# Optimization experiments

Hardware: AMD Instinct MI355X
Metric: run time of the kernel (lower is better)

## Reference

```python
import jax, jax.numpy as jnp
import numpy as np

N_NODES = 500_000
MEM_DIM = 256
MSG_DIM = 256
N_UPD = 100_000


def setup_inputs() -> dict:
    key = jax.random.key(0)
    ks = jax.random.split(key, 10)
    s = 1.0 / np.sqrt(MEM_DIM)
    return {
        "unique_node_ids": jnp.arange(N_UPD, dtype=jnp.int64)
        if jax.config.jax_enable_x64 else jnp.arange(N_UPD, dtype=jnp.int32),
        "unique_messages": jax.random.normal(ks[0], (N_UPD, MSG_DIM), jnp.float32),
        "timestamps": jax.random.uniform(ks[1], (N_UPD,), jnp.float32),
        "net_transaction_amounts": jax.random.normal(ks[2], (N_UPD,), jnp.float32),
        "memory": jax.random.normal(ks[3], (N_NODES, MEM_DIM), jnp.float32),
        "last_update": jnp.zeros((N_NODES,), jnp.float32),
        "W_cat": jax.random.normal(ks[4], (MEM_DIM, MSG_DIM + 1), jnp.float32) * s,
        "b_cat": jnp.zeros((MEM_DIM,), jnp.float32),
        "W_ih": jax.random.normal(ks[5], (3 * MEM_DIM, MEM_DIM), jnp.float32) * s,
        "W_hh": jax.random.normal(ks[6], (3 * MEM_DIM, MEM_DIM), jnp.float32) * s,
        "b_ih": jnp.zeros((3 * MEM_DIM,), jnp.float32),
        "b_hh": jnp.zeros((3 * MEM_DIM,), jnp.float32),
    }


def _gru_cell(x, h, W_ih, W_hh, b_ih, b_hh):
    # torch.nn.GRUCell math
    gi = x @ W_ih.T + b_ih      # [N, 3*D]
    gh = h @ W_hh.T + b_hh      # [N, 3*D]
    i_r, i_z, i_n = jnp.split(gi, 3, axis=1)
    h_r, h_z, h_n = jnp.split(gh, 3, axis=1)
    r = jax.nn.sigmoid(i_r + h_r)
    z = jax.nn.sigmoid(i_z + h_z)
    n = jnp.tanh(i_n + r * h_n)
    return (1.0 - z) * n + z * h


def reference(unique_node_ids, unique_messages, timestamps, net_transaction_amounts,
              memory, last_update, W_cat, b_cat, W_ih, W_hh, b_ih, b_hh):
    # concat message with scalar amount, small linear projection
    cat = jnp.concatenate([unique_messages, net_transaction_amounts[:, None]], axis=1)
    final_inputs = cat @ W_cat.T + b_cat                # [N_upd, MEM_DIM]
    h = memory[unique_node_ids]                         # gather by id
    new_h = _gru_cell(final_inputs, h, W_ih, W_hh, b_ih, b_hh)
    updated_memory = memory.at[unique_node_ids].set(new_h)        # scatter back
    updated_last_update = last_update.at[unique_node_ids].set(timestamps)
    return updated_memory, updated_last_update
```

## Files before the change

kernel.cpp:

```cpp
#include <hip/hip_runtime.h>
#include <hip/hip_bf16.h>

typedef __attribute__((ext_vector_type(8))) short s16x8;
typedef __attribute__((ext_vector_type(4))) float f32x4;

__device__ __forceinline__ unsigned short f2bf(float x) {
    unsigned int u = __float_as_uint(x);
    u += 0x7fffu + ((u >> 16) & 1u);
    return (unsigned short)(u >> 16);
}
__device__ __forceinline__ float bf2f(unsigned short h) {
    return __uint_as_float((unsigned int)h << 16);
}
__device__ __forceinline__ void gload_lds16(const void* g, void* l) {
    __builtin_amdgcn_global_load_lds(
        (const __attribute__((address_space(1))) void*)g,
        (__attribute__((address_space(3))) void*)(unsigned int)(size_t)l,
        16, 0, 0);
}

__global__ void prep_w_kernel(const float* __restrict__ W_cat,
                              const float* __restrict__ b_cat,
                              const float* __restrict__ W_ih,
                              const float* __restrict__ W_hh,
                              const float* __restrict__ b_ih,
                              unsigned short* __restrict__ wm,
                              unsigned short* __restrict__ whh,
                              float* __restrict__ wamt,
                              float* __restrict__ bcomb) {
    int idx = blockIdx.x * blockDim.x + threadIdx.x;
    const int NW = 768 * 256;
    if (idx < NW) {
        int g = idx >> 8, c = idx & 255;
        float s = 0.f;
        #pragma unroll 4
        for (int k = 0; k < 256; ++k) s += W_ih[g * 256 + k] * W_cat[k * 257 + c];
        wm[idx] = f2bf(s);
    } else if (idx < 2 * NW) {
        int t = idx - NW;
        whh[t] = f2bf(W_hh[t]);
    } else if (idx < 2 * NW + 768) {
        int g = idx - 2 * NW;
        float sa = 0.f, sb = 0.f;
        for (int k = 0; k < 256; ++k) {
            float w = W_ih[g * 256 + k];
            sa += w * W_cat[k * 257 + 256];
            sb += w * b_cat[k];
        }
        wamt[g] = sa;
        bcomb[g] = sb + b_ih[g];
    }
}

__global__ void prep_msgs_kernel(const float* __restrict__ msgs,
                                 unsigned short* __restrict__ mbf,
                                 const float* __restrict__ lu,
                                 float* __restrict__ out_lu,
                                 long mchunks, long luchunks) {
    long stride = (long)gridDim.x * blockDim.x;
    long total = mchunks + luchunks;
    for (long i = blockIdx.x * (long)blockDim.x + threadIdx.x; i < total; i += stride) {
        if (i < mchunks) {
            const float4* s = (const float4*)(msgs + i * 8);
            float4 a = s[0], b = s[1];
            s16x8 v = { (short)f2bf(a.x), (short)f2bf(a.y), (short)f2bf(a.z), (short)f2bf(a.w),
                        (short)f2bf(b.x), (short)f2bf(b.y), (short)f2bf(b.z), (short)f2bf(b.w) };
            *(s16x8*)(mbf + i * 8) = v;
        } else {
            long j = i - mchunks;
            ((float4*)out_lu)[j] = ((const float4*)lu)[j];
        }
    }
}

__global__ void build_inv_kernel(const int* __restrict__ ids, int* __restrict__ inv, int M) {
    int i = blockIdx.x * blockDim.x + threadIdx.x;
    if (i < M) inv[ids[i]] = i + 1;
}

template<bool HBF>
__global__ void copy_gather_kernel(const float* __restrict__ memory,
                                   const int* __restrict__ inv,
                                   float* __restrict__ out_mem,
                                   unsigned short* __restrict__ hbf,
                                   int N) {
    int wave = (blockIdx.x * blockDim.x + threadIdx.x) >> 6;
    int lane = threadIdx.x & 63;
    int nw = (gridDim.x * blockDim.x) >> 6;
    for (int row = wave; row < N; row += nw) {
        int iv = inv[row];
        if (iv == 0) {
            float4 v = ((const float4*)(memory + (size_t)row * 256))[lane];
            ((float4*)(out_mem + (size_t)row * 256))[lane] = v;
        } else if (HBF) {
            float4 v = ((const float4*)(memory + (size_t)row * 256))[lane];
            ushort4 o = { f2bf(v.x), f2bf(v.y), f2bf(v.z), f2bf(v.w) };
            *(ushort4*)(hbf + (size_t)(iv - 1) * 256 + lane * 4) = o;
        }
    }
}

__device__ __forceinline__ void stage_dma_a(const unsigned short* __restrict__ base,
                                            int m0, int M, int k0, char* ldsbuf, int tid) {
    #pragma unroll
    for (int it = 0; it < 2; ++it) {
        int q = tid + it * 512;
        int row = q >> 3;
        int part = (q & 7) ^ (row & 7);
        int grow = m0 + row; if (grow >= M) grow = M - 1;
        gload_lds16((const char*)base + (size_t)grow * 512 + k0 * 2 + part * 16,
                    ldsbuf + (tid & ~63) * 16 + it * 8192);
    }
}
__device__ __forceinline__ void stage_dma_w(const unsigned short* __restrict__ wm,
                                            const unsigned short* __restrict__ whh,
                                            int nc, int k0, char* swbuf, int tid) {
    #pragma unroll
    for (int it = 0; it < 6; ++it) {
        int q = tid + it * 512;
        int r = q >> 3;
        int part = (q & 7) ^ (r & 7);
        int pn = r >> 6, rr = r & 63;
        const unsigned short* src = (pn < 3)
            ? wm  + ((size_t)(pn * 256 + nc * 64 + rr)) * 256
            : whh + ((size_t)((pn - 3) * 256 + nc * 64 + rr)) * 256;
        gload_lds16((const char*)src + k0 * 2 + part * 16,
                    swbuf + (tid & ~63) * 16 + it * 8192);
    }
}
__device__ __forceinline__ void stage_reg_h(const int* __restrict__ ids,
                                            const float* __restrict__ memory,
                                            int m0, int M, int k0, char* shbuf, int tid) {
    #pragma unroll
    for (int it = 0; it < 2; ++it) {
        int q = tid + it * 512;
        int row = q >> 3, part = q & 7;
        int grow = m0 + row; if (grow >= M) grow = M - 1;
        int gid = ids[grow];
        const float4* src = (const float4*)(memory + (size_t)gid * 256 + k0 + part * 8);
        float4 a = src[0], b = src[1];
        s16x8 v = { (short)f2bf(a.x), (short)f2bf(a.y), (short)f2bf(a.z), (short)f2bf(a.w),
                    (short)f2bf(b.x), (short)f2bf(b.y), (short)f2bf(b.z), (short)f2bf(b.w) };
        *(s16x8*)(shbuf + row * 128 + ((part ^ (row & 7)) * 16)) = v;
    }
}

template<bool HBF>
__global__ __launch_bounds__(512, 2)
void gru_kernel(const int* __restrict__ ids,
                const unsigned short* __restrict__ mbf,
                const unsigned short* __restrict__ hbf,
                const float* __restrict__ memory,
                const unsigned short* __restrict__ wm,
                const unsigned short* __restrict__ whh,
                const float* __restrict__ wamt,
                const float* __restrict__ bcomb,
                const float* __restrict__ b_hh,
                const float* __restrict__ amt,
                const float* __restrict__ ts,
                float* __restrict__ out_mem,
                float* __restrict__ out_lu,
                int M, int mtiles) {
    extern __shared__ char lds[];

    int g = blockIdx.x;
    int xcd = g & 7, s = g >> 3;
    int nc = s & 3;
    int mtile = (s >> 2) * 8 + xcd;
    if (mtile >= mtiles) return;
    int m0 = mtile * 128;

    int tid = threadIdx.x;
    int lane = tid & 63;
    int w = tid >> 6;
    int wr = w >> 2, wc = w & 3;

    stage_dma_a(mbf, m0, M, 0, lds, tid);
    if (HBF) stage_dma_a(hbf, m0, M, 0, lds + 32768, tid);
    else     stage_reg_h(ids, memory, m0, M, 0, lds + 32768, tid);
    stage_dma_w(wm, whh, nc, 0, lds + 65536, tid);
    __syncthreads();

    f32x4 acc[6][4];
    #pragma unroll
    for (int pn = 0; pn < 6; ++pn)
        #pragma unroll
        for (int mf = 0; mf < 4; ++mf) acc[pn][mf] = (f32x4){0.f, 0.f, 0.f, 0.f};

    #pragma unroll
    for (int ks = 0; ks < 4; ++ks) {
        char* sm = lds + ((ks & 1) << 14);
        char* sh = lds + 32768 + ((ks & 1) << 14);
        char* sw = lds + 65536 + (ks & 1) * 49152;
        if (ks < 3) {
            int k0 = (ks + 1) * 64;
            char* smn = lds + (((ks + 1) & 1) << 14);
            char* shn = lds + 32768 + (((ks + 1) & 1) << 14);
            char* swn = lds + 65536 + ((ks + 1) & 1) * 49152;
            stage_dma_a(mbf, m0, M, k0, smn, tid);
            if (HBF) stage_dma_a(hbf, m0, M, k0, shn, tid);
            else     stage_reg_h(ids, memory, m0, M, k0, shn, tid);
            stage_dma_w(wm, whh, nc, k0, swn, tid);
        }
        #pragma unroll
        for (int c = 0; c < 2; ++c) {
            int p = c * 4 + (lane >> 4);
            s16x8 ax[4], ah[4], bw[6];
            #pragma unroll
            for (int mf = 0; mf < 4; ++mf) {
                int row = wr * 64 + mf * 16 + (lane & 15);
                int off = row * 128 + ((p ^ (row & 7)) * 16);
                ax[mf] = *(const s16x8*)(sm + off);
                ah[mf] = *(const s16x8*)(sh + off);
            }
            #pragma unroll
            for (int pn = 0; pn < 6; ++pn) {
                int r = pn * 64 + wc * 16 + (lane & 15);
                bw[pn] = *(const s16x8*)(sw + r * 128 + ((p ^ (r & 7)) * 16));
            }
            #pragma unroll
            for (int pn = 0; pn < 6; ++pn)
                #pragma unroll
                for (int mf = 0; mf < 4; ++mf)
                    acc[pn][mf] = __builtin_amdgcn_mfma_f32_16x16x32_bf16(
                        (pn < 3) ? ax[mf] : ah[mf], bw[pn], acc[pn][mf], 0, 0, 0);
        }
        __syncthreads();
    }

    int colL = wc * 16 + (lane & 15);
    int col = nc * 64 + colL;
    float bi0 = bcomb[col], bi1 = bcomb[256 + col], bi2 = bcomb[512 + col];
    float bh0 = b_hh[col],  bh1 = b_hh[256 + col],  bh2 = b_hh[512 + col];
    float wa0 = wamt[col],  wa1 = wamt[256 + col],  wa2 = wamt[512 + col];
    bool lu_thread = (nc == 0) && (colL == 0);
    #pragma unroll
    for (int mf = 0; mf < 4; ++mf) {
        int rb = wr * 64 + mf * 16 + (lane >> 4) * 4;
        #pragma unroll
        for (int r = 0; r < 4; ++r) {
            int grow = m0 + rb + r; if (grow >= M) grow = M - 1;
            int gid = ids[grow];
            float amtv = amt[grow];
            float hv = HBF ? bf2f(hbf[(size_t)grow * 256 + col])
                           : memory[(size_t)gid * 256 + col];
            float ir = acc[0][mf][r] + bi0 + amtv * wa0;
            float iz = acc[1][mf][r] + bi1 + amtv * wa1;
            float in_ = acc[2][mf][r] + bi2 + amtv * wa2;
            float hr = acc[3][mf][r] + bh0;
            float hz = acc[4][mf][r] + bh1;
            float hn = acc[5][mf][r] + bh2;
            float rg = 1.f / (1.f + __expf(-(ir + hr)));
            float zg = 1.f / (1.f + __expf(-(iz + hz)));
            float ng = tanhf(in_ + rg * hn);
            out_mem[(size_t)gid * 256 + col] = (1.f - zg) * ng + zg * hv;
            if (lu_thread) out_lu[gid] = ts[grow];
        }
    }
}

extern "C" void kernel_launch(void* const* d_in, const int* in_sizes, int n_in,
                              void* d_out, int out_size, void* d_ws, size_t ws_size,
                              hipStream_t stream) {
    const int*   ids   = (const int*)  d_in[0];
    const float* msgs  = (const float*)d_in[1];
    const float* ts    = (const float*)d_in[2];
    const float* amt   = (const float*)d_in[3];
    const float* mem   = (const float*)d_in[4];
    const float* lu    = (const float*)d_in[5];
    const float* W_cat = (const float*)d_in[6];
    const float* b_cat = (const float*)d_in[7];
    const float* W_ih  = (const float*)d_in[8];
    const float* W_hh  = (const float*)d_in[9];
    const float* b_ih  = (const float*)d_in[10];
    const float* b_hh  = (const float*)d_in[11];

    int M = in_sizes[0];
    int N = in_sizes[5];

    float* out_mem = (float*)d_out;
    float* out_lu  = out_mem + (size_t)N * 256;

    char* ws = (char*)d_ws;
    unsigned short* wm    = (unsigned short*)ws;
    unsigned short* whh   = wm + 768 * 256;
    float*          wamt  = (float*)(whh + 768 * 256);
    float*          bcomb = wamt + 768;
    int*            inv   = (int*)(bcomb + 768);
    size_t off_mbf = (((char*)(inv + N) - ws) + 15) & ~(size_t)15;
    unsigned short* mbf   = (unsigned short*)(ws + off_mbf);
    unsigned short* hbf   = (unsigned short*)(ws + off_mbf + (size_t)M * 512);
    size_t need_hbf = off_mbf + 2 * (size_t)M * 512;
    bool use_hbf = ws_size >= need_hbf;

    prep_w_kernel<<<(2 * 768 * 256 + 768 + 255) / 256, 256, 0, stream>>>(
        W_cat, b_cat, W_ih, W_hh, b_ih, wm, whh, wamt, bcomb);

    long mchunks = (long)M * 32;
    long luchunks = N / 4;
    prep_msgs_kernel<<<2048, 256, 0, stream>>>(msgs, mbf, lu, out_lu, mchunks, luchunks);

    (void)hipMemsetAsync(inv, 0, (size_t)N * 4, stream);
    build_inv_kernel<<<(M + 255) / 256, 256, 0, stream>>>(ids, inv, M);

    int mtiles = (M + 127) / 128;
    int mt8 = ((mtiles + 7) / 8) * 8;

    if (use_hbf) {
        copy_gather_kernel<true><<<2048, 256, 0, stream>>>(mem, inv, out_mem, hbf, N);
        (void)hipFuncSetAttribute((const void*)gru_kernel<true>,
                                  hipFuncAttributeMaxDynamicSharedMemorySize, 163840);
        gru_kernel<true><<<mt8 * 4, 512, 163840, stream>>>(
            ids, mbf, hbf, mem, wm, whh, wamt, bcomb, b_hh, amt, ts,
            out_mem, out_lu, M, mtiles);
    } else {
        copy_gather_kernel<false><<<2048, 256, 0, stream>>>(mem, inv, out_mem, hbf, N);
        (void)hipFuncSetAttribute((const void*)gru_kernel<false>,
                                  hipFuncAttributeMaxDynamicSharedMemorySize, 163840);
        gru_kernel<false><<<mt8 * 4, 512, 163840, stream>>>(
            ids, mbf, hbf, mem, wm, whh, wamt, bcomb, b_hh, amt, ts,
            out_mem, out_lu, M, mtiles);
    }
}
```

Measured before the change: 454.8 us.

## Fuse bf16 conversion into GRU kernel loads and drop bf16 staging buffers

Removes the separate message and hidden-state bf16 pre-conversion passes (prep_msgs and the hbf write in copy_gather). The GRU kernel now loads fp32 messages and gathered memory rows directly into registers, converts them, and writes them to single-buffered LDS between two barriers, while weights keep the DMA double buffer. The copy of untouched rows and the last_update write move to a copy kernel that runs after the GRU kernel, with 4-way unrolled row loads. A cheaper exp-based tanh replaces tanhf. This cuts a full extra round trip through HBM for the staged bf16 arrays, at the cost of an extra barrier per k-step and less load/compute overlap for the activation tiles.

```diff
diff --git a/kernel.cpp b/kernel.cpp
--- a/kernel.cpp
+++ b/kernel.cpp
@@ -9,14 +9,19 @@
     u += 0x7fffu + ((u >> 16) & 1u);
     return (unsigned short)(u >> 16);
 }
-__device__ __forceinline__ float bf2f(unsigned short h) {
-    return __uint_as_float((unsigned int)h << 16);
+__device__ __forceinline__ s16x8 pack8(float4 a, float4 b) {
+    return (s16x8){ (short)f2bf(a.x), (short)f2bf(a.y), (short)f2bf(a.z), (short)f2bf(a.w),
+                    (short)f2bf(b.x), (short)f2bf(b.y), (short)f2bf(b.z), (short)f2bf(b.w) };
 }
 __device__ __forceinline__ void gload_lds16(const void* g, void* l) {
     __builtin_amdgcn_global_load_lds(
         (const __attribute__((address_space(1))) void*)g,
         (__attribute__((address_space(3))) void*)(unsigned int)(size_t)l,
         16, 0, 0);
+}
+__device__ __forceinline__ float sigf(float x) { return 1.f / (1.f + __expf(-x)); }
+__device__ __forceinline__ float tanhfast(float x) {
+    return 1.f - 2.f / (__expf(2.f * x) + 1.f);
 }
 
 __global__ void prep_w_kernel(const float* __restrict__ W_cat,
@@ -52,69 +57,14 @@
     }
 }
 
-__global__ void prep_msgs_kernel(const float* __restrict__ msgs,
-                                 unsigned short* __restrict__ mbf,
-                                 const float* __restrict__ lu,
-                                 float* __restrict__ out_lu,
-                                 long mchunks, long luchunks) {
-    long stride = (long)gridDim.x * blockDim.x;
-    long total = mchunks + luchunks;
-    for (long i = blockIdx.x * (long)blockDim.x + threadIdx.x; i < total; i += stride) {
-        if (i < mchunks) {
-            const float4* s = (const float4*)(msgs + i * 8);
-            float4 a = s[0], b = s[1];
-            s16x8 v = { (short)f2bf(a.x), (short)f2bf(a.y), (short)f2bf(a.z), (short)f2bf(a.w),
-                        (short)f2bf(b.x), (short)f2bf(b.y), (short)f2bf(b.z), (short)f2bf(b.w) };
-            *(s16x8*)(mbf + i * 8) = v;
-        } else {
-            long j = i - mchunks;
-            ((float4*)out_lu)[j] = ((const float4*)lu)[j];
-        }
-    }
-}
-
 __global__ void build_inv_kernel(const int* __restrict__ ids, int* __restrict__ inv, int M) {
     int i = blockIdx.x * blockDim.x + threadIdx.x;
     if (i < M) inv[ids[i]] = i + 1;
 }
 
-template<bool HBF>
-__global__ void copy_gather_kernel(const float* __restrict__ memory,
-                                   const int* __restrict__ inv,
-                                   float* __restrict__ out_mem,
-                                   unsigned short* __restrict__ hbf,
-                                   int N) {
-    int wave = (blockIdx.x * blockDim.x + threadIdx.x) >> 6;
-    int lane = threadIdx.x & 63;
-    int nw = (gridDim.x * blockDim.x) >> 6;
-    for (int row = wave; row < N; row += nw) {
-        int iv = inv[row];
-        if (iv == 0) {
-            float4 v = ((const float4*)(memory + (size_t)row * 256))[lane];
-            ((float4*)(out_mem + (size_t)row * 256))[lane] = v;
-        } else if (HBF) {
-            float4 v = ((const float4*)(memory + (size_t)row * 256))[lane];
-            ushort4 o = { f2bf(v.x), f2bf(v.y), f2bf(v.z), f2bf(v.w) };
-            *(ushort4*)(hbf + (size_t)(iv - 1) * 256 + lane * 4) = o;
-        }
-    }
-}
-
-__device__ __forceinline__ void stage_dma_a(const unsigned short* __restrict__ base,
-                                            int m0, int M, int k0, char* ldsbuf, int tid) {
-    #pragma unroll
-    for (int it = 0; it < 2; ++it) {
-        int q = tid + it * 512;
-        int row = q >> 3;
-        int part = (q & 7) ^ (row & 7);
-        int grow = m0 + row; if (grow >= M) grow = M - 1;
-        gload_lds16((const char*)base + (size_t)grow * 512 + k0 * 2 + part * 16,
-                    ldsbuf + (tid & ~63) * 16 + it * 8192);
-    }
-}
-__device__ __forceinline__ void stage_dma_w(const unsigned short* __restrict__ wm,
-                                            const unsigned short* __restrict__ whh,
-                                            int nc, int k0, char* swbuf, int tid) {
+__device__ __forceinline__ void dma_w(const unsigned short* __restrict__ wm,
+                                      const unsigned short* __restrict__ whh,
+                                      int nc, int k0, char* swbuf, int tid) {
     #pragma unroll
     for (int it = 0; it < 6; ++it) {
         int q = tid + it * 512;
@@ -128,28 +78,10 @@
                     swbuf + (tid & ~63) * 16 + it * 8192);
     }
 }
-__device__ __forceinline__ void stage_reg_h(const int* __restrict__ ids,
-                                            const float* __restrict__ memory,
-                                            int m0, int M, int k0, char* shbuf, int tid) {
-    #pragma unroll
-    for (int it = 0; it < 2; ++it) {
-        int q = tid + it * 512;
-        int row = q >> 3, part = q & 7;
-        int grow = m0 + row; if (grow >= M) grow = M - 1;
-        int gid = ids[grow];
-        const float4* src = (const float4*)(memory + (size_t)gid * 256 + k0 + part * 8);
-        float4 a = src[0], b = src[1];
-        s16x8 v = { (short)f2bf(a.x), (short)f2bf(a.y), (short)f2bf(a.z), (short)f2bf(a.w),
-                    (short)f2bf(b.x), (short)f2bf(b.y), (short)f2bf(b.z), (short)f2bf(b.w) };
-        *(s16x8*)(shbuf + row * 128 + ((part ^ (row & 7)) * 16)) = v;
-    }
-}
-
-template<bool HBF>
+
 __global__ __launch_bounds__(512, 2)
 void gru_kernel(const int* __restrict__ ids,
-                const unsigned short* __restrict__ mbf,
-                const unsigned short* __restrict__ hbf,
+                const float* __restrict__ msgs,
                 const float* __restrict__ memory,
                 const unsigned short* __restrict__ wm,
                 const unsigned short* __restrict__ whh,
@@ -157,11 +89,13 @@
                 const float* __restrict__ bcomb,
                 const float* __restrict__ b_hh,
                 const float* __restrict__ amt,
-                const float* __restrict__ ts,
                 float* __restrict__ out_mem,
-                float* __restrict__ out_lu,
                 int M, int mtiles) {
     extern __shared__ char lds[];
+    char* sm  = lds;
+    char* sh  = lds + 16384;
+    char* sw0 = lds + 32768;
+    char* sw1 = lds + 81920;
 
     int g = blockIdx.x;
     int xcd = g & 7, s = g >> 3;
@@ -175,10 +109,29 @@
     int w = tid >> 6;
     int wr = w >> 2, wc = w & 3;
 
-    stage_dma_a(mbf, m0, M, 0, lds, tid);
-    if (HBF) stage_dma_a(hbf, m0, M, 0, lds + 32768, tid);
-    else     stage_reg_h(ids, memory, m0, M, 0, lds + 32768, tid);
-    stage_dma_w(wm, whh, nc, 0, lds + 65536, tid);
+    int row0 = tid >> 3, row1 = (tid + 512) >> 3;
+    int part = tid & 7;
+    int gr0 = m0 + row0; if (gr0 >= M) gr0 = M - 1;
+    int gr1 = m0 + row1; if (gr1 >= M) gr1 = M - 1;
+    const float* mp0 = msgs + (size_t)gr0 * 256 + part * 8;
+    const float* mp1 = msgs + (size_t)gr1 * 256 + part * 8;
+    const float* hp0 = memory + (size_t)ids[gr0] * 256 + part * 8;
+    const float* hp1 = memory + (size_t)ids[gr1] * 256 + part * 8;
+    int ld0 = row0 * 128 + ((part ^ (row0 & 7)) * 16);
+    int ld1 = row1 * 128 + ((part ^ (row1 & 7)) * 16);
+
+    float4 ma0, mb0, ma1, mb1, ha0, hb0, ha1, hb1;
+    {
+        ma0 = *(const float4*)(mp0);     mb0 = *(const float4*)(mp0 + 4);
+        ma1 = *(const float4*)(mp1);     mb1 = *(const float4*)(mp1 + 4);
+        ha0 = *(const float4*)(hp0);     hb0 = *(const float4*)(hp0 + 4);
+        ha1 = *(const float4*)(hp1);     hb1 = *(const float4*)(hp1 + 4);
+        dma_w(wm, whh, nc, 0, sw0, tid);
+        *(s16x8*)(sm + ld0) = pack8(ma0, mb0);
+        *(s16x8*)(sm + ld1) = pack8(ma1, mb1);
+        *(s16x8*)(sh + ld0) = pack8(ha0, hb0);
+        *(s16x8*)(sh + ld1) = pack8(ha1, hb1);
+    }
     __syncthreads();
 
     f32x4 acc[6][4];
@@ -189,18 +142,14 @@
 
     #pragma unroll
     for (int ks = 0; ks < 4; ++ks) {
-        char* sm = lds + ((ks & 1) << 14);
-        char* sh = lds + 32768 + ((ks & 1) << 14);
-        char* sw = lds + 65536 + (ks & 1) * 49152;
+        char* swc = (ks & 1) ? sw1 : sw0;
         if (ks < 3) {
             int k0 = (ks + 1) * 64;
-            char* smn = lds + (((ks + 1) & 1) << 14);
-            char* shn = lds + 32768 + (((ks + 1) & 1) << 14);
-            char* swn = lds + 65536 + ((ks + 1) & 1) * 49152;
-            stage_dma_a(mbf, m0, M, k0, smn, tid);
-            if (HBF) stage_dma_a(hbf, m0, M, k0, shn, tid);
-            else     stage_reg_h(ids, memory, m0, M, k0, shn, tid);
-            stage_dma_w(wm, whh, nc, k0, swn, tid);
+            ma0 = *(const float4*)(mp0 + k0);  mb0 = *(const float4*)(mp0 + k0 + 4);
+            ma1 = *(const float4*)(mp1 + k0);  mb1 = *(const float4*)(mp1 + k0 + 4);
+            ha0 = *(const float4*)(hp0 + k0);  hb0 = *(const float4*)(hp0 + k0 + 4);
+            ha1 = *(const float4*)(hp1 + k0);  hb1 = *(const float4*)(hp1 + k0 + 4);
+            dma_w(wm, whh, nc, k0, (ks & 1) ? sw0 : sw1, tid);
         }
         #pragma unroll
         for (int c = 0; c < 2; ++c) {
@@ -216,7 +165,7 @@
             #pragma unroll
             for (int pn = 0; pn < 6; ++pn) {
                 int r = pn * 64 + wc * 16 + (lane & 15);
-                bw[pn] = *(const s16x8*)(sw + r * 128 + ((p ^ (r & 7)) * 16));
+                bw[pn] = *(const s16x8*)(swc + r * 128 + ((p ^ (r & 7)) * 16));
             }
             #pragma unroll
             for (int pn = 0; pn < 6; ++pn)
@@ -225,7 +174,14 @@
                     acc[pn][mf] = __builtin_amdgcn_mfma_f32_16x16x32_bf16(
                         (pn < 3) ? ax[mf] : ah[mf], bw[pn], acc[pn][mf], 0, 0, 0);
         }
-        __syncthreads();
+        if (ks < 3) {
+            __syncthreads();
+            *(s16x8*)(sm + ld0) = pack8(ma0, mb0);
+            *(s16x8*)(sm + ld1) = pack8(ma1, mb1);
+            *(s16x8*)(sh + ld0) = pack8(ha0, hb0);
+            *(s16x8*)(sh + ld1) = pack8(ha1, hb1);
+            __syncthreads();
+        }
     }
 
     int colL = wc * 16 + (lane & 15);
@@ -233,7 +189,6 @@
     float bi0 = bcomb[col], bi1 = bcomb[256 + col], bi2 = bcomb[512 + col];
     float bh0 = b_hh[col],  bh1 = b_hh[256 + col],  bh2 = b_hh[512 + col];
     float wa0 = wamt[col],  wa1 = wamt[256 + col],  wa2 = wamt[512 + col];
-    bool lu_thread = (nc == 0) && (colL == 0);
     #pragma unroll
     for (int mf = 0; mf < 4; ++mf) {
         int rb = wr * 64 + mf * 16 + (lane >> 4) * 4;
@@ -242,20 +197,53 @@
             int grow = m0 + rb + r; if (grow >= M) grow = M - 1;
             int gid = ids[grow];
             float amtv = amt[grow];
-            float hv = HBF ? bf2f(hbf[(size_t)grow * 256 + col])
-                           : memory[(size_t)gid * 256 + col];
+            float hv = memory[(size_t)gid * 256 + col];
             float ir = acc[0][mf][r] + bi0 + amtv * wa0;
             float iz = acc[1][mf][r] + bi1 + amtv * wa1;
             float in_ = acc[2][mf][r] + bi2 + amtv * wa2;
             float hr = acc[3][mf][r] + bh0;
             float hz = acc[4][mf][r] + bh1;
             float hn = acc[5][mf][r] + bh2;
-            float rg = 1.f / (1.f + __expf(-(ir + hr)));
-            float zg = 1.f / (1.f + __expf(-(iz + hz)));
-            float ng = tanhf(in_ + rg * hn);
+            float rg = sigf(ir + hr);
+            float zg = sigf(iz + hz);
+            float ng = tanhfast(in_ + rg * hn);
             out_mem[(size_t)gid * 256 + col] = (1.f - zg) * ng + zg * hv;
-            if (lu_thread) out_lu[gid] = ts[grow];
-        }
+        }
+    }
+}
+
+__global__ __launch_bounds__(256)
+void copy_kernel(const float* __restrict__ memory,
+                 const int* __restrict__ inv,
+                 const float* __restrict__ lu,
+                 const float* __restrict__ ts,
+                 float* __restrict__ out_mem,
+                 float* __restrict__ out_lu,
+                 int N) {
+    int wid = (blockIdx.x * blockDim.x + threadIdx.x) >> 6;
+    int lane = threadIdx.x & 63;
+    int nw = (gridDim.x * blockDim.x) >> 6;
+    for (int base = wid; base < N; base += nw * 4) {
+        int  r0 = base, r1 = base + nw, r2 = base + 2 * nw, r3 = base + 3 * nw;
+        bool d0 = (r0 < N) && (inv[r0] == 0);
+        bool d1 = (r1 < N) && (inv[r1] == 0);
+        bool d2 = (r2 < N) && (inv[r2] == 0);
+        bool d3 = (r3 < N) && (inv[r3] == 0);
+        float4 v0, v1, v2, v3;
+        if (d0) v0 = ((const float4*)(memory + (size_t)r0 * 256))[lane];
+        if (d1) v1 = ((const float4*)(memory + (size_t)r1 * 256))[lane];
+        if (d2) v2 = ((const float4*)(memory + (size_t)r2 * 256))[lane];
+        if (d3) v3 = ((const float4*)(memory + (size_t)r3 * 256))[lane];
+        if (d0) ((float4*)(out_mem + (size_t)r0 * 256))[lane] = v0;
+        if (d1) ((float4*)(out_mem + (size_t)r1 * 256))[lane] = v1;
+        if (d2) ((float4*)(out_mem + (size_t)r2 * 256))[lane] = v2;
+        if (d3) ((float4*)(out_mem + (size_t)r3 * 256))[lane] = v3;
+    }
+    int gidx = blockIdx.x * blockDim.x + threadIdx.x;
+    int stride = gridDim.x * blockDim.x;
+    for (int i = gidx; i < N; i += stride) {
+        int iv = inv[i];
+        out_lu[i] = iv ? ts[iv - 1] : lu[i];
     }
 }
 
@@ -287,38 +275,19 @@
     float*          wamt  = (float*)(whh + 768 * 256);
     float*          bcomb = wamt + 768;
     int*            inv   = (int*)(bcomb + 768);
-    size_t off_mbf = (((char*)(inv + N) - ws) + 15) & ~(size_t)15;
-    unsigned short* mbf   = (unsigned short*)(ws + off_mbf);
-    unsigned short* hbf   = (unsigned short*)(ws + off_mbf + (size_t)M * 512);
-    size_t need_hbf = off_mbf + 2 * (size_t)M * 512;
-    bool use_hbf = ws_size >= need_hbf;
 
     prep_w_kernel<<<(2 * 768 * 256 + 768 + 255) / 256, 256, 0, stream>>>(
         W_cat, b_cat, W_ih, W_hh, b_ih, wm, whh, wamt, bcomb);
 
-    long mchunks = (long)M * 32;
-    long luchunks = N / 4;
-    prep_msgs_kernel<<<2048, 256, 0, stream>>>(msgs, mbf, lu, out_lu, mchunks, luchunks);
-
     (void)hipMemsetAsync(inv, 0, (size_t)N * 4, stream);
     build_inv_kernel<<<(M + 255) / 256, 256, 0, stream>>>(ids, inv, M);
 
     int mtiles = (M + 127) / 128;
     int mt8 = ((mtiles + 7) / 8) * 8;
-
-    if (use_hbf) {
-        copy_gather_kernel<true><<<2048, 256, 0, stream>>>(mem, inv, out_mem, hbf, N);
-        (void)hipFuncSetAttribute((const void*)gru_kernel<true>,
-                                  hipFuncAttributeMaxDynamicSharedMemorySize, 163840);
-        gru_kernel<true><<<mt8 * 4, 512, 163840, stream>>>(
-            ids, mbf, hbf, mem, wm, whh, wamt, bcomb, b_hh, amt, ts,
-            out_mem, out_lu, M, mtiles);
-    } else {
-        copy_gather_kernel<false><<<2048, 256, 0, stream>>>(mem, inv, out_mem, hbf, N);
-        (void)hipFuncSetAttribute((const void*)gru_kernel<false>,
-                                  hipFuncAttributeMaxDynamicSharedMemorySize, 163840);
-        gru_kernel<false><<<mt8 * 4, 512, 163840, stream>>>(
-            ids, mbf, hbf, mem, wm, whh, wamt, bcomb, b_hh, amt, ts,
-            out_mem, out_lu, M, mtiles);
-    }
-}
+    (void)hipFuncSetAttribute((const void*)gru_kernel,
+                              hipFuncAttributeMaxDynamicSharedMemorySize, 131072);
+    gru_kernel<<<mt8 * 4, 512, 131072, stream>>>(
+        ids, msgs, mem, wm, whh, wamt, bcomb, b_hh, amt, out_mem, M, mtiles);
+
+    copy_kernel<<<2048, 256, 0, stream>>>(mem, inv, lu, ts, out_mem, out_lu, N);
+}
```

Measured after the change: 422.0 us. -7.2%, faster.
